# Optimization experiments

Hardware: AMD Instinct MI355X
Metric: run time of the kernel (lower is better)

## Reference

```python
import jax, jax.numpy as jnp
import numpy as np

S, B, C = 7, 2, 20
EPS = 1e-6
LAMBDA_COORD = 5.0
LAMBDA_NOOBJ = 0.5


def setup_inputs() -> dict:
    key = jax.random.key(0)
    k1, k2 = jax.random.split(key)
    N = 16384
    p = jax.random.uniform(k1, (N, S, S, B * 5 + C), dtype=jnp.float32)
    a = jax.random.uniform(k2, (N, S, S, B * 5 + C), dtype=jnp.float32)
    return {"p": p, "a": a}


def _attr(t, i):
    # i-th attribute of each of the B boxes: channels C+i, C+i+5, ... -> [N,S,S,B]
    return t[..., C + i::5]


def _coords(t):
    x, y, w, h = _attr(t, 0), _attr(t, 1), _attr(t, 2), _attr(t, 3)
    tl = jnp.stack((x - w / 2.0, y - h / 2.0), axis=-1)  # [N,S,S,B,2]
    br = jnp.stack((x + w / 2.0, y + h / 2.0), axis=-1)
    return tl, br


def _sse(x, y):
    return jnp.sum((x - y) ** 2)


def reference(p, a):
    # pairwise IoU between predicted boxes (axis 3) and target boxes (axis 4)
    p_tl, p_br = _coords(p)
    a_tl, a_br = _coords(a)
    tl = jnp.maximum(p_tl[:, :, :, :, None, :], a_tl[:, :, :, None, :, :])  # [N,S,S,B,B,2]
    br = jnp.minimum(p_br[:, :, :, :, None, :], a_br[:, :, :, None, :, :])
    sides = jnp.clip(br - tl, 0.0)
    inter = sides[..., 0] * sides[..., 1]  # [N,S,S,B,B]
    p_area = (_attr(p, 2) * _attr(p, 3))[:, :, :, :, None]
    a_area = (_attr(a, 2) * _attr(a, 3))[:, :, :, None, :]
    union = p_area + a_area - inter
    zero_union = union == 0.0
    iou = jnp.where(zero_union, 0.0, inter) / jnp.where(zero_union, EPS, union)
    max_iou = jnp.max(iou, axis=-1)  # [N,S,S,B]

    obj_i = (_attr(a, 4) > 0.0)[..., 0:1]  # [N,S,S,1]
    responsible = jnp.argmax(max_iou, axis=-1, keepdims=True) == jnp.arange(B)  # [N,S,S,B]
    obj_ij = (obj_i & responsible).astype(p.dtype)
    noobj_ij = 1.0 - obj_ij

    loss_x = _sse(obj_ij * _attr(a, 0), obj_ij * _attr(p, 0))
    loss_y = _sse(obj_ij * _attr(a, 1), obj_ij * _attr(p, 1))
    loss_w = _sse(obj_ij * jnp.sign(_attr(a, 2)) * jnp.sqrt(_attr(a, 2) + EPS),
                  obj_ij * jnp.sign(_attr(p, 2)) * jnp.sqrt(_attr(p, 2) + EPS))
    loss_h = _sse(obj_ij * jnp.sign(_attr(a, 3)) * jnp.sqrt(_attr(a, 3) + EPS),
                  obj_ij * jnp.sign(_attr(p, 3)) * jnp.sqrt(_attr(p, 3) + EPS))
    loss_conf_obj = _sse(obj_ij * obj_ij, obj_ij * _attr(p, 4))
    loss_conf_noobj = _sse(noobj_ij * obj_ij, noobj_ij * _attr(p, 4))
    obj_if = obj_i.astype(p.dtype)
    cls_loss = _sse(obj_if * p[..., 5 * B:], obj_if * a[..., 5 * B:])

    return (LAMBDA_COORD * (loss_x + loss_y + loss_w + loss_h)
            + loss_conf_obj + LAMBDA_NOOBJ * loss_conf_noobj + cls_loss)
```

## Files before the change

### kernel.cpp

```cpp
#include <hip/hip_runtime.h>


#define CH    30
#define EPSL  1e-6f
#define TPB   256
#define REGION_F   (TPB * CH)
#define REGION_F4  (REGION_F / 4)

typedef const __attribute__((address_space(1))) void* gas_ptr;
typedef __attribute__((address_space(3))) void* las_ptr;

__device__ __forceinline__ float sgnf(float x) {
    return (x > 0.0f) ? 1.0f : ((x < 0.0f) ? -1.0f : 0.0f);
}

__global__ __launch_bounds__(TPB, 5) void yolo_loss_kernel(const float* __restrict__ p,
                                                           const float* __restrict__ a,
                                                           float* __restrict__ out,
                                                           long long n_cells) {
    __shared__ float lds[REGION_F];
    __shared__ float wsum[TPB / 64];

    const int tid  = threadIdx.x;
    const int wid  = tid >> 6;
    const int lane = tid & 63;
    const long long cell0 = (long long)blockIdx.x * TPB;
    const long long cell  = cell0 + tid;
    const bool full   = (cell0 + TPB) <= n_cells;
    const bool active = cell < n_cells;

    float pd[20], ad[20];
    float lsum = 0.0f;

    if (full) {
        {
            const float* gbase = p + cell0 * CH;
#pragma unroll
            for (int k = 0; k < 8; ++k) {
                const int b4 = k * TPB + wid * 64;
                if (b4 < REGION_F4) {
                    __builtin_amdgcn_global_load_lds(
                        (gas_ptr)(gbase + (size_t)(b4 + lane) * 4),
                        (las_ptr)(lds + (size_t)b4 * 4),
                        16, 0, 0);
                }
            }
        }
        __syncthreads();
#pragma unroll
        for (int i = 0; i < 10; ++i) {
            const float2 v = *(const float2*)(lds + tid * CH + 10 + 2 * i);
            pd[2 * i] = v.x; pd[2 * i + 1] = v.y;
        }
        __syncthreads();

        {
            const float* gbase = a + cell0 * CH;
#pragma unroll
            for (int k = 0; k < 8; ++k) {
                const int b4 = k * TPB + wid * 64;
                if (b4 < REGION_F4) {
                    __builtin_amdgcn_global_load_lds(
                        (gas_ptr)(gbase + (size_t)(b4 + lane) * 4),
                        (las_ptr)(lds + (size_t)b4 * 4),
                        16, 0, 0);
                }
            }
        }
        __syncthreads();
#pragma unroll
        for (int i = 0; i < 10; ++i) {
            const float2 v = *(const float2*)(lds + tid * CH + 10 + 2 * i);
            ad[2 * i] = v.x; ad[2 * i + 1] = v.y;
        }
    } else if (active) {
        const float2* cp2 = (const float2*)(p + cell * CH + 10);
        const float2* ca2 = (const float2*)(a + cell * CH + 10);
#pragma unroll
        for (int i = 0; i < 10; ++i) {
            const float2 v = cp2[i];
            pd[2 * i] = v.x; pd[2 * i + 1] = v.y;
        }
#pragma unroll
        for (int i = 0; i < 10; ++i) {
            const float2 v = ca2[i];
            ad[2 * i] = v.x; ad[2 * i + 1] = v.y;
        }
    }

    if (active) {
        float pxv[2], pyv[2], pwv[2], phv[2], pcv[2];
        float axv[2], ayv[2], awv[2], ahv[2];
#pragma unroll
        for (int b = 0; b < 2; ++b) {
            pxv[b] = pd[10 + 5 * b]; pyv[b] = pd[11 + 5 * b];
            pwv[b] = pd[12 + 5 * b]; phv[b] = pd[13 + 5 * b];
            pcv[b] = pd[14 + 5 * b];
            axv[b] = ad[10 + 5 * b]; ayv[b] = ad[11 + 5 * b];
            awv[b] = ad[12 + 5 * b]; ahv[b] = ad[13 + 5 * b];
        }
        const bool obj = ad[14] > 0.0f;

        float miou[2];
#pragma unroll
        for (int pb = 0; pb < 2; ++pb) {
            const float p_tlx = pxv[pb] - 0.5f * pwv[pb];
            const float p_tly = pyv[pb] - 0.5f * phv[pb];
            const float p_brx = pxv[pb] + 0.5f * pwv[pb];
            const float p_bry = pyv[pb] + 0.5f * phv[pb];
            const float p_area = pwv[pb] * phv[pb];
            float best = -3.4e38f;
#pragma unroll
            for (int ab = 0; ab < 2; ++ab) {
                const float a_tlx = axv[ab] - 0.5f * awv[ab];
                const float a_tly = ayv[ab] - 0.5f * ahv[ab];
                const float a_brx = axv[ab] + 0.5f * awv[ab];
                const float a_bry = ayv[ab] + 0.5f * ahv[ab];
                float sx = fminf(p_brx, a_brx) - fmaxf(p_tlx, a_tlx);
                float sy = fminf(p_bry, a_bry) - fmaxf(p_tly, a_tly);
                sx = fmaxf(sx, 0.0f);
                sy = fmaxf(sy, 0.0f);
                const float inter = sx * sy;
                const float uni = p_area + awv[ab] * ahv[ab] - inter;
                const float iou = (uni == 0.0f) ? 0.0f : (inter / uni);
                best = fmaxf(best, iou);
            }
            miou[pb] = best;
        }
        const int resp = (miou[1] > miou[0]) ? 1 : 0;

#pragma unroll
        for (int b = 0; b < 2; ++b) {
            const bool oij = obj && (b == resp);
            if (oij) {
                const float dx = axv[b] - pxv[b];
                const float dy = ayv[b] - pyv[b];
                const float dw = sgnf(awv[b]) * sqrtf(awv[b] + EPSL) - sgnf(pwv[b]) * sqrtf(pwv[b] + EPSL);
                const float dh = sgnf(ahv[b]) * sqrtf(ahv[b] + EPSL) - sgnf(phv[b]) * sqrtf(phv[b] + EPSL);
                const float dc = 1.0f - pcv[b];
                lsum += 5.0f * (dx * dx + dy * dy + dw * dw + dh * dh) + dc * dc;
            } else {
                lsum += 0.5f * pcv[b] * pcv[b];
            }
        }

        if (obj) {
#pragma unroll
            for (int k = 0; k < 20; ++k) {
                const float d = pd[k] - ad[k];
                lsum += d * d;
            }
        }
    }

    float v = lsum;
#pragma unroll
    for (int off = 32; off > 0; off >>= 1)
        v += __shfl_down(v, off, 64);
    if ((tid & 63) == 0) wsum[tid >> 6] = v;
    __syncthreads();
    if (tid == 0) {
        float t = 0.0f;
#pragma unroll
        for (int w = 0; w < TPB / 64; ++w) t += wsum[w];
        atomicAdd(out, t);
    }
}

extern "C" void kernel_launch(void* const* d_in, const int* in_sizes, int n_in,
                              void* d_out, int out_size, void* d_ws, size_t ws_size,
                              hipStream_t stream) {
    const float* p = (const float*)d_in[0];
    const float* a = (const float*)d_in[1];
    float* out = (float*)d_out;

    const long long n_cells = (long long)in_sizes[0] / CH;
    const int grid = (int)((n_cells + TPB - 1) / TPB);

    hipMemsetAsync(d_out, 0, sizeof(float), stream);
    yolo_loss_kernel<<<grid, TPB, 0, stream>>>(p, a, out, n_cells);
}
```

Baseline: 206.8 us.

## Persistent grid with double-buffered LDS staging of p and a tiles

Replaces one block per 256-cell tile with a fixed grid of 512 blocks of 128 threads that loop over tiles. Each iteration asynchronously stages the next tile of both p and a into a second LDS buffer with global_load_lds while the current tile is computed. This removes the serial load-sync-read pattern and the repeated block launches, and cuts the number of atomic adds. In exchange each block holds about 61KB of LDS and runs only two waves, so occupancy is low. Correctness also depends on the barrier waiting for the async LDS loads to finish.

```diff
diff --git a/kernel.cpp b/kernel.cpp
--- a/kernel.cpp
+++ b/kernel.cpp
@@ -1,11 +1,13 @@
 #include <hip/hip_runtime.h>
 
 
-#define CH    30
-#define EPSL  1e-6f
-#define TPB   256
-#define REGION_F   (TPB * CH)
-#define REGION_F4  (REGION_F / 4)
+#define CH      30
+#define EPSL    1e-6f
+#define TPB     128
+#define TILE_F  (TPB * CH)
+#define TILE_F4 (TILE_F / 4)
+#define BUF_F   (2 * TILE_F)
+#define GRID    512
 
 typedef const __attribute__((address_space(1))) void* gas_ptr;
 typedef __attribute__((address_space(3))) void* las_ptr;
@@ -14,142 +16,160 @@
     return (x > 0.0f) ? 1.0f : ((x < 0.0f) ? -1.0f : 0.0f);
 }
 
-__global__ __launch_bounds__(TPB, 5) void yolo_loss_kernel(const float* __restrict__ p,
-                                                           const float* __restrict__ a,
-                                                           float* __restrict__ out,
-                                                           long long n_cells) {
-    __shared__ float lds[REGION_F];
+__device__ __forceinline__ void stage_tile(const float* __restrict__ p,
+                                           const float* __restrict__ a,
+                                           float* buf, long long tile,
+                                           int wid, int lane) {
+    const float* gp = p + tile * (long long)TILE_F;
+    const float* ga = a + tile * (long long)TILE_F;
+#pragma unroll
+    for (int k = 0; k < 8; ++k) {
+        const int b4 = k * TPB + wid * 64;
+        if (b4 < TILE_F4) {
+            __builtin_amdgcn_global_load_lds(
+                (gas_ptr)(gp + (size_t)(b4 + lane) * 4),
+                (las_ptr)(buf + (size_t)b4 * 4), 16, 0, 0);
+        }
+    }
+#pragma unroll
+    for (int k = 0; k < 8; ++k) {
+        const int b4 = k * TPB + wid * 64;
+        if (b4 < TILE_F4) {
+            __builtin_amdgcn_global_load_lds(
+                (gas_ptr)(ga + (size_t)(b4 + lane) * 4),
+                (las_ptr)(buf + TILE_F + (size_t)b4 * 4), 16, 0, 0);
+        }
+    }
+}
+
+__device__ __forceinline__ float cell_loss(const float* pd, const float* ad) {
+    float lsum = 0.0f;
+
+    float pxv[2], pyv[2], pwv[2], phv[2], pcv[2];
+    float axv[2], ayv[2], awv[2], ahv[2];
+#pragma unroll
+    for (int b = 0; b < 2; ++b) {
+        pxv[b] = pd[10 + 5 * b]; pyv[b] = pd[11 + 5 * b];
+        pwv[b] = pd[12 + 5 * b]; phv[b] = pd[13 + 5 * b];
+        pcv[b] = pd[14 + 5 * b];
+        axv[b] = ad[10 + 5 * b]; ayv[b] = ad[11 + 5 * b];
+        awv[b] = ad[12 + 5 * b]; ahv[b] = ad[13 + 5 * b];
+    }
+    const bool obj = ad[14] > 0.0f;
+
+    float miou[2];
+#pragma unroll
+    for (int pb = 0; pb < 2; ++pb) {
+        const float p_tlx = pxv[pb] - 0.5f * pwv[pb];
+        const float p_tly = pyv[pb] - 0.5f * phv[pb];
+        const float p_brx = pxv[pb] + 0.5f * pwv[pb];
+        const float p_bry = pyv[pb] + 0.5f * phv[pb];
+        const float p_area = pwv[pb] * phv[pb];
+        float best = -3.4e38f;
+#pragma unroll
+        for (int ab = 0; ab < 2; ++ab) {
+            const float a_tlx = axv[ab] - 0.5f * awv[ab];
+            const float a_tly = ayv[ab] - 0.5f * ahv[ab];
+            const float a_brx = axv[ab] + 0.5f * awv[ab];
+            const float a_bry = ayv[ab] + 0.5f * ahv[ab];
+            float sx = fminf(p_brx, a_brx) - fmaxf(p_tlx, a_tlx);
+            float sy = fminf(p_bry, a_bry) - fmaxf(p_tly, a_tly);
+            sx = fmaxf(sx, 0.0f);
+            sy = fmaxf(sy, 0.0f);
+            const float inter = sx * sy;
+            const float uni = p_area + awv[ab] * ahv[ab] - inter;
+            const float iou = (uni == 0.0f) ? 0.0f : (inter / uni);
+            best = fmaxf(best, iou);
+        }
+        miou[pb] = best;
+    }
+    const int resp = (miou[1] > miou[0]) ? 1 : 0;
+
+#pragma unroll
+    for (int b = 0; b < 2; ++b) {
+        const bool oij = obj && (b == resp);
+        if (oij) {
+            const float dx = axv[b] - pxv[b];
+            const float dy = ayv[b] - pyv[b];
+            const float dw = sgnf(awv[b]) * sqrtf(awv[b] + EPSL) - sgnf(pwv[b]) * sqrtf(pwv[b] + EPSL);
+            const float dh = sgnf(ahv[b]) * sqrtf(ahv[b] + EPSL) - sgnf(phv[b]) * sqrtf(phv[b] + EPSL);
+            const float dc = 1.0f - pcv[b];
+            lsum += 5.0f * (dx * dx + dy * dy + dw * dw + dh * dh) + dc * dc;
+        } else {
+            lsum += 0.5f * pcv[b] * pcv[b];
+        }
+    }
+
+    if (obj) {
+#pragma unroll
+        for (int k = 0; k < 20; ++k) {
+            const float d = pd[k] - ad[k];
+            lsum += d * d;
+        }
+    }
+    return lsum;
+}
+
+__global__ __launch_bounds__(TPB) void yolo_loss_kernel(const float* __restrict__ p,
+                                                        const float* __restrict__ a,
+                                                        float* __restrict__ out,
+                                                        long long n_cells) {
+    __shared__ float lds[2][BUF_F];
     __shared__ float wsum[TPB / 64];
 
     const int tid  = threadIdx.x;
     const int wid  = tid >> 6;
     const int lane = tid & 63;
-    const long long cell0 = (long long)blockIdx.x * TPB;
-    const long long cell  = cell0 + tid;
-    const bool full   = (cell0 + TPB) <= n_cells;
-    const bool active = cell < n_cells;
-
-    float pd[20], ad[20];
+    const long long FT = n_cells / TPB;
+    const int nb = gridDim.x;
+
     float lsum = 0.0f;
-
-    if (full) {
-        {
-            const float* gbase = p + cell0 * CH;
-#pragma unroll
-            for (int k = 0; k < 8; ++k) {
-                const int b4 = k * TPB + wid * 64;
-                if (b4 < REGION_F4) {
-                    __builtin_amdgcn_global_load_lds(
-                        (gas_ptr)(gbase + (size_t)(b4 + lane) * 4),
-                        (las_ptr)(lds + (size_t)b4 * 4),
-                        16, 0, 0);
-                }
+    long long t = blockIdx.x;
+    int cur = 0;
+
+    if (t < FT) stage_tile(p, a, lds[0], t, wid, lane);
+    __syncthreads();
+
+    for (; t < FT; t += nb) {
+        const long long tn = t + nb;
+        if (tn < FT) stage_tile(p, a, lds[cur ^ 1], tn, wid, lane);
+
+        float pd[20], ad[20];
+        const float* bp = lds[cur] + tid * CH + 10;
+        const float* ba = lds[cur] + TILE_F + tid * CH + 10;
+#pragma unroll
+        for (int i = 0; i < 10; ++i) {
+            const float2 v = *(const float2*)(bp + 2 * i);
+            pd[2 * i] = v.x; pd[2 * i + 1] = v.y;
+        }
+#pragma unroll
+        for (int i = 0; i < 10; ++i) {
+            const float2 v = *(const float2*)(ba + 2 * i);
+            ad[2 * i] = v.x; ad[2 * i + 1] = v.y;
+        }
+        lsum += cell_loss(pd, ad);
+
+        __syncthreads();
+        cur ^= 1;
+    }
+
+    if (blockIdx.x == 0) {
+        const long long c = FT * TPB + tid;
+        if (c < n_cells) {
+            float pd[20], ad[20];
+            const float2* cp2 = (const float2*)(p + c * CH + 10);
+            const float2* ca2 = (const float2*)(a + c * CH + 10);
+#pragma unroll
+            for (int i = 0; i < 10; ++i) {
+                const float2 v = cp2[i];
+                pd[2 * i] = v.x; pd[2 * i + 1] = v.y;
             }
-        }
-        __syncthreads();
-#pragma unroll
-        for (int i = 0; i < 10; ++i) {
-            const float2 v = *(const float2*)(lds + tid * CH + 10 + 2 * i);
-            pd[2 * i] = v.x; pd[2 * i + 1] = v.y;
-        }
-        __syncthreads();
-
-        {
-            const float* gbase = a + cell0 * CH;
-#pragma unroll
-            for (int k = 0; k < 8; ++k) {
-                const int b4 = k * TPB + wid * 64;
-                if (b4 < REGION_F4) {
-                    __builtin_amdgcn_global_load_lds(
-                        (gas_ptr)(gbase + (size_t)(b4 + lane) * 4),
-                        (las_ptr)(lds + (size_t)b4 * 4),
-                        16, 0, 0);
-                }
+#pragma unroll
+            for (int i = 0; i < 10; ++i) {
+                const float2 v = ca2[i];
+                ad[2 * i] = v.x; ad[2 * i + 1] = v.y;
             }
-        }
-        __syncthreads();
-#pragma unroll
-        for (int i = 0; i < 10; ++i) {
-            const float2 v = *(const float2*)(lds + tid * CH + 10 + 2 * i);
-            ad[2 * i] = v.x; ad[2 * i + 1] = v.y;
-        }
-    } else if (active) {
-        const float2* cp2 = (const float2*)(p + cell * CH + 10);
-        const float2* ca2 = (const float2*)(a + cell * CH + 10);
-#pragma unroll
-        for (int i = 0; i < 10; ++i) {
-            const float2 v = cp2[i];
-            pd[2 * i] = v.x; pd[2 * i + 1] = v.y;
-        }
-#pragma unroll
-        for (int i = 0; i < 10; ++i) {
-            const float2 v = ca2[i];
-            ad[2 * i] = v.x; ad[2 * i + 1] = v.y;
-        }
-    }
-
-    if (active) {
-        float pxv[2], pyv[2], pwv[2], phv[2], pcv[2];
-        float axv[2], ayv[2], awv[2], ahv[2];
-#pragma unroll
-        for (int b = 0; b < 2; ++b) {
-            pxv[b] = pd[10 + 5 * b]; pyv[b] = pd[11 + 5 * b];
-            pwv[b] = pd[12 + 5 * b]; phv[b] = pd[13 + 5 * b];
-            pcv[b] = pd[14 + 5 * b];
-            axv[b] = ad[10 + 5 * b]; ayv[b] = ad[11 + 5 * b];
-            awv[b] = ad[12 + 5 * b]; ahv[b] = ad[13 + 5 * b];
-        }
-        const bool obj = ad[14] > 0.0f;
-
-        float miou[2];
-#pragma unroll
-        for (int pb = 0; pb < 2; ++pb) {
-            const float p_tlx = pxv[pb] - 0.5f * pwv[pb];
-            const float p_tly = pyv[pb] - 0.5f * phv[pb];
-            const float p_brx = pxv[pb] + 0.5f * pwv[pb];
-            const float p_bry = pyv[pb] + 0.5f * phv[pb];
-            const float p_area = pwv[pb] * phv[pb];
-            float best = -3.4e38f;
-#pragma unroll
-            for (int ab = 0; ab < 2; ++ab) {
-                const float a_tlx = axv[ab] - 0.5f * awv[ab];
-                const float a_tly = ayv[ab] - 0.5f * ahv[ab];
-                const float a_brx = axv[ab] + 0.5f * awv[ab];
-                const float a_bry = ayv[ab] + 0.5f * ahv[ab];
-                float sx = fminf(p_brx, a_brx) - fmaxf(p_tlx, a_tlx);
-                float sy = fminf(p_bry, a_bry) - fmaxf(p_tly, a_tly);
-                sx = fmaxf(sx, 0.0f);
-                sy = fmaxf(sy, 0.0f);
-                const float inter = sx * sy;
-                const float uni = p_area + awv[ab] * ahv[ab] - inter;
-                const float iou = (uni == 0.0f) ? 0.0f : (inter / uni);
-                best = fmaxf(best, iou);
-            }
-            miou[pb] = best;
-        }
-        const int resp = (miou[1] > miou[0]) ? 1 : 0;
-
-#pragma unroll
-        for (int b = 0; b < 2; ++b) {
-            const bool oij = obj && (b == resp);
-            if (oij) {
-                const float dx = axv[b] - pxv[b];
-                const float dy = ayv[b] - pyv[b];
-                const float dw = sgnf(awv[b]) * sqrtf(awv[b] + EPSL) - sgnf(pwv[b]) * sqrtf(pwv[b] + EPSL);
-                const float dh = sgnf(ahv[b]) * sqrtf(ahv[b] + EPSL) - sgnf(phv[b]) * sqrtf(phv[b] + EPSL);
-                const float dc = 1.0f - pcv[b];
-                lsum += 5.0f * (dx * dx + dy * dy + dw * dw + dh * dh) + dc * dc;
-            } else {
-                lsum += 0.5f * pcv[b] * pcv[b];
-            }
-        }
-
-        if (obj) {
-#pragma unroll
-            for (int k = 0; k < 20; ++k) {
-                const float d = pd[k] - ad[k];
-                lsum += d * d;
-            }
+            lsum += cell_loss(pd, ad);
         }
     }
 
@@ -160,10 +180,10 @@
     if ((tid & 63) == 0) wsum[tid >> 6] = v;
     __syncthreads();
     if (tid == 0) {
-        float t = 0.0f;
-#pragma unroll
-        for (int w = 0; w < TPB / 64; ++w) t += wsum[w];
-        atomicAdd(out, t);
+        float t2 = 0.0f;
+#pragma unroll
+        for (int w = 0; w < TPB / 64; ++w) t2 += wsum[w];
+        atomicAdd(out, t2);
     }
 }
 
@@ -175,8 +195,7 @@
     float* out = (float*)d_out;
 
     const long long n_cells = (long long)in_sizes[0] / CH;
-    const int grid = (int)((n_cells + TPB - 1) / TPB);
 
     hipMemsetAsync(d_out, 0, sizeof(float), stream);
-    yolo_loss_kernel<<<grid, TPB, 0, stream>>>(p, a, out, n_cells);
-}
+    yolo_loss_kernel<<<GRID, TPB, 0, stream>>>(p, a, out, n_cells);
+}
```

Result: slower. 211.6 us (+2.4%).
